# Optimization experiments

Hardware: AMD Instinct MI355X
Metric: run time of the kernel (lower is better)

## Reference

```python
import jax, jax.numpy as jnp
import numpy as np

NUM_Q_HEADS = 32
NUM_KV_HEADS = 8
HEAD_DIM = 128
ROPE_THETA = 10000.0
Q_SIZE = NUM_Q_HEADS * HEAD_DIM      # 4096
KV_SIZE = NUM_KV_HEADS * HEAD_DIM    # 1024


def _apply_rope_neox(x, positions, theta=ROPE_THETA):
    # x: [T, H, D]; neox-style rotate-halves RoPE
    T, H, D = x.shape
    half = D // 2
    inv_freq = 1.0 / (theta ** (jnp.arange(half, dtype=jnp.float32) / half))
    freqs = positions.astype(jnp.float32)[:, None] * inv_freq[None, :]  # [T, half]
    cos = jnp.cos(freqs)[:, None, :]  # [T, 1, half]
    sin = jnp.sin(freqs)[:, None, :]
    x1, x2 = x[..., :half], x[..., half:]
    return jnp.concatenate([x1 * cos - x2 * sin, x2 * cos + x1 * sin], axis=-1).astype(x.dtype)


def setup_inputs() -> dict:
    key = jax.random.key(0)
    k1, k2, k3 = jax.random.split(key, 3)
    T, E = 8192, 4096
    hidden_states = jax.random.normal(k1, (T, E), dtype=jnp.float32) * 0.02
    positions = jnp.arange(T, dtype=jnp.int32)
    w_qkv = jax.random.normal(k2, (E, Q_SIZE + 2 * KV_SIZE), dtype=jnp.float32) * 0.02
    w_o = jax.random.normal(k3, (Q_SIZE, E), dtype=jnp.float32) * 0.02
    return {"hidden_states": hidden_states, "positions": positions, "w_qkv": w_qkv, "w_o": w_o}


def reference(hidden_states, positions, w_qkv, w_o):
    T = hidden_states.shape[0]
    qkv = hidden_states @ w_qkv                              # [T, 6144]
    q = qkv[:, :Q_SIZE].reshape(T, NUM_Q_HEADS, HEAD_DIM)
    k = qkv[:, Q_SIZE:Q_SIZE + KV_SIZE].reshape(T, NUM_KV_HEADS, HEAD_DIM)
    v = qkv[:, Q_SIZE + KV_SIZE:]                            # [T, KV_SIZE] (unused by stub)
    q = _apply_rope_neox(q, positions)
    k = _apply_rope_neox(k, positions)
    # Attention is stubbed in the source (randn_like(q)); we use the RoPE'd q
    # as the deterministic stand-in so the pipeline stays reproducible.
    attn_output = q.reshape(T, Q_SIZE)
    output = attn_output @ w_o                               # [T, 4096]
    return output
```

## Files before the change

### kernel.cpp

```cpp
#include <hip/hip_runtime.h>
#include <hip/hip_bf16.h>
#include <stdint.h>

#define T_DIM 8192
#define E_DIM 4096
#define NQH   32
#define HD    128
#define QSZ   (NQH * HD)
#define QKV_COLS 6144

typedef unsigned short u16;
typedef __attribute__((ext_vector_type(8))) short   bf16x8;
typedef __attribute__((ext_vector_type(4))) float   f32x4;
typedef __attribute__((ext_vector_type(4))) unsigned short u16x4;

__device__ __forceinline__ u16 f2bf(float f) {
    uint32_t u = __float_as_uint(f);
    u += 0x7fffu + ((u >> 16) & 1u);
    return (u16)(u >> 16);
}
__device__ __forceinline__ float bf2f(u16 u) {
    return __uint_as_float(((uint32_t)u) << 16);
}

__device__ __forceinline__ void gload_lds16(u16* lds, const u16* g) {
    __builtin_amdgcn_global_load_lds(
        (const __attribute__((address_space(1))) uint32_t*)g,
        (__attribute__((address_space(3))) uint32_t*)lds,
        16, 0, 0);
}

__global__ void convert_f32_bf16(const float* __restrict__ in, u16* __restrict__ out, size_t n4) {
    size_t i = (size_t)blockIdx.x * blockDim.x + threadIdx.x;
    size_t stride = (size_t)gridDim.x * blockDim.x;
    for (; i < n4; i += stride) {
        float4 v = ((const float4*)in)[i];
        u16x4 o;
        o.x = f2bf(v.x); o.y = f2bf(v.y); o.z = f2bf(v.z); o.w = f2bf(v.w);
        ((u16x4*)out)[i] = o;
    }
}

__global__ void transpose_conv(const float* __restrict__ W, u16* __restrict__ Wt,
                               int K, int N, int ldW, int colOff) {
    __shared__ float tile[32][33];
    const int tx = threadIdx.x, ty = threadIdx.y;
    const int n0 = blockIdx.x * 32, k0 = blockIdx.y * 32;
#pragma unroll
    for (int j = 0; j < 4; ++j) {
        int k = k0 + ty + j * 8;
        tile[ty + j * 8][tx] = W[(size_t)k * ldW + colOff + n0 + tx];
    }
    __syncthreads();
#pragma unroll
    for (int j = 0; j < 4; ++j) {
        int n = n0 + ty + j * 8;
        Wt[(size_t)n * K + k0 + tx] = f2bf(tile[tx][ty + j * 8]);
    }
}

__global__ void rope_table(const int* __restrict__ pos, float2* __restrict__ tab) {
    int idx = blockIdx.x * blockDim.x + threadIdx.x;
    int t = idx >> 6, d = idx & 63;
    float inv = powf(10000.0f, -(float)d * (1.0f / 64.0f));
    float fr  = (float)pos[t] * inv;
    float s, c;
    sincosf(fr, &s, &c);
    tab[idx] = make_float2(c, s);
}

__device__ __forceinline__ void store_out(u16* p, float v)  { *p = f2bf(v); }
__device__ __forceinline__ void store_out(float* p, float v){ *p = v; }

#define VMC(N)  asm volatile("s_waitcnt vmcnt(%0)"  :: "n"(N) : "memory")
#define LGKM(N) asm volatile("s_waitcnt lgkmcnt(%0)" :: "n"(N) : "memory")
#define PHASE_SYNC() do { __builtin_amdgcn_sched_barrier(0); __builtin_amdgcn_s_barrier(); \
                          LGKM(0); __builtin_amdgcn_sched_barrier(0); } while (0)
#define ENDBAR() do { __builtin_amdgcn_sched_barrier(0); __builtin_amdgcn_s_barrier(); } while (0)

#define STG_A(buf, h, kOff) do { \
    const u16* s_ = sA + (size_t)(h) * 128 * K + (kOff); \
    u16* d_ = dL + (buf) * 32768 + (h) * 8192; \
    gload_lds16(d_, s_); gload_lds16(d_ + 4096, s_ + (size_t)64 * K); } while (0)
#define STG_B(buf, h, kOff) do { \
    const u16* s_ = sB + (size_t)(h) * 128 * K + (kOff); \
    u16* d_ = dL + 16384 + (buf) * 32768 + (h) * 8192; \
    gload_lds16(d_, s_); gload_lds16(d_ + 4096, s_ + (size_t)64 * K); } while (0)

#define RD_A(buf, miBase, d0, d1) do { _Pragma("unroll") \
    for (int m = 0; m < 4; ++m) { \
        const u16* p_ = lds + (buf) * 32768 + wm * 8192 + ((miBase) + m) * 1024 + aRow; \
        d0[m] = *(const bf16x8*)(p_ + cOf0); \
        d1[m] = *(const bf16x8*)(p_ + cOf1); } } while (0)
#define RD_B(buf, niBase, d0, d1) do { _Pragma("unroll") \
    for (int n = 0; n < 2; ++n) { \
        const int ni_ = (niBase) + n; \
        const u16* p_ = lds + (buf) * 32768 + 16384 + (ni_ >> 1) * 8192 + \
                        ((ni_ & 1) * 64 + wn * 16) * 64 + aRow; \
        d0[n] = *(const bf16x8*)(p_ + cOf0); \
        d1[n] = *(const bf16x8*)(p_ + cOf1); } } while (0)

#define MM(miBase, niBase, A0, A1, B0, B1) do { \
    __builtin_amdgcn_s_setprio(1); \
    _Pragma("unroll") for (int m = 0; m < 4; ++m) \
    _Pragma("unroll") for (int n = 0; n < 2; ++n) { \
        acc[(miBase) + m][(niBase) + n] = __builtin_amdgcn_mfma_f32_16x16x32_bf16( \
            A0[m], B0[n], acc[(miBase) + m][(niBase) + n], 0, 0, 0); \
        acc[(miBase) + m][(niBase) + n] = __builtin_amdgcn_mfma_f32_16x16x32_bf16( \
            A1[m], B1[n], acc[(miBase) + m][(niBase) + n], 0, 0, 0); } \
    __builtin_amdgcn_s_setprio(0); } while (0)

#define TILE(BUF, KN) do {                                                     \
                                                                  \
    RD_A(BUF, 0, a0K0, a0K1);                                                  \
    RD_B(BUF, 0, b01K0, b01K1);                                                \
    STG_A((BUF) ^ 1, 0, KN);                                                   \
    LGKM(8);                                                                   \
    PHASE_SYNC();                                                              \
    MM(0, 0, a0K0, a0K1, b01K0, b01K1);                                        \
    ENDBAR();                                                                  \
                                                                  \
    RD_A(BUF, 4, a4K0, a4K1);                                                  \
    STG_A((BUF) ^ 1, 1, KN);                                                   \
    VMC(4);                                                                    \
    PHASE_SYNC();                                                              \
    MM(4, 0, a4K0, a4K1, b01K0, b01K1);                                        \
    ENDBAR();                                                                  \
                                                                  \
    RD_B(BUF, 2, b23K0, b23K1);                                                \
    STG_B((BUF) ^ 1, 0, KN);                                                   \
    PHASE_SYNC();                                                              \
    MM(0, 2, a0K0, a0K1, b23K0, b23K1);                                        \
    ENDBAR();                                                                  \
                                                                  \
    STG_B((BUF) ^ 1, 1, KN);                                                   \
    VMC(2);                                                                    \
    PHASE_SYNC();                                                              \
    MM(4, 2, a4K0, a4K1, b23K0, b23K1);                                        \
    ENDBAR();                                                                  \
  } while (0)

template <typename OutT, bool ROPE>
__global__ __launch_bounds__(512, 2) void gemm256(const u16* __restrict__ A,
                                                  const u16* __restrict__ Bt,
                                                  OutT* __restrict__ C,
                                                  const float2* __restrict__ tab,
                                                  int M, int N, int K) {
    __shared__ u16 lds[65536];
    const int tid  = threadIdx.x;
    const int lane = tid & 63;
    const int wid  = tid >> 6;
    const int wm = wid >> 2;
    const int wn = wid & 3;
    const int lr  = lane & 15;
    const int kq  = lane >> 4;
    const int lr7 = lr & 7;
    const int aRow = lr * 64;
    const int cOf0 = ((kq) ^ lr7) << 3;
    const int cOf1 = ((4 + kq) ^ lr7) << 3;

    const int nwg = gridDim.x;
    const int cpx = nwg >> 3;
    const int bid = blockIdx.x;
    const int swz = (bid & 7) * cpx + (bid >> 3);
    const int numM = M >> 8;
    const size_t rowBase = (size_t)(swz % numM) << 8;
    const size_t colBase = (size_t)(swz / numM) << 8;

    const int r0 = tid >> 3;
    const int cS = (((tid & 7) ^ (r0 & 7)) << 3);
    const u16* sA = A  + (rowBase + r0) * (size_t)K + cS;
    const u16* sB = Bt + (colBase + r0) * (size_t)K + cS;
    u16* dL = &lds[0] + tid * 8;

    f32x4 acc[8][4];
#pragma unroll
    for (int i = 0; i < 8; ++i)
#pragma unroll
        for (int j = 0; j < 4; ++j)
            acc[i][j] = (f32x4){0.f, 0.f, 0.f, 0.f};

    bf16x8 a0K0[4], a0K1[4], a4K0[4], a4K1[4];
    bf16x8 b01K0[2], b01K1[2], b23K0[2], b23K1[2];

    STG_A(0, 0, 0); STG_A(0, 1, 0); STG_B(0, 0, 0);
    STG_B(0, 1, 0);
    VMC(2);
    __builtin_amdgcn_sched_barrier(0);
    __builtin_amdgcn_s_barrier();
    __builtin_amdgcn_sched_barrier(0);

    const int nT = K >> 6;
    for (int t = 0; t < nT; t += 2) {
        const int kN1 = (t + 1) << 6;
        const int kN2 = (t + 2 < nT) ? ((t + 2) << 6) : 0;
        TILE(0, kN1);
        TILE(1, kN2);
    }
    VMC(0);

    if constexpr (ROPE) {
        const int dIdx = wn * 16 + lr;
#pragma unroll
        for (int mi = 0; mi < 8; ++mi)
#pragma unroll
            for (int r = 0; r < 4; ++r) {
                size_t row = rowBase + wm * 128 + mi * 16 + (kq << 2) + r;
                float2 cs = tab[row * 64 + dIdx];
#pragma unroll
                for (int hp = 0; hp < 2; ++hp) {
                    float x1 = acc[mi][hp * 2 + 0][r];
                    float x2 = acc[mi][hp * 2 + 1][r];
                    size_t c1 = colBase + hp * 128 + wn * 16 + lr;
                    C[row * (size_t)N + c1]      = f2bf(x1 * cs.x - x2 * cs.y);
                    C[row * (size_t)N + c1 + 64] = f2bf(x2 * cs.x + x1 * cs.y);
                }
            }
    } else {
#pragma unroll
        for (int mi = 0; mi < 8; ++mi)
#pragma unroll
            for (int ni = 0; ni < 4; ++ni)
#pragma unroll
                for (int r = 0; r < 4; ++r) {
                    size_t row = rowBase + wm * 128 + mi * 16 + (kq << 2) + r;
                    size_t col = colBase + ni * 64 + wn * 16 + lr;
                    store_out(&C[row * (size_t)N + col], acc[mi][ni][r]);
                }
    }
}

extern "C" void kernel_launch(void* const* d_in, const int* in_sizes, int n_in,
                              void* d_out, int out_size, void* d_ws, size_t ws_size,
                              hipStream_t stream) {
    const float* hidden    = (const float*)d_in[0];
    const int*   positions = (const int*)d_in[1];
    const float* w_qkv     = (const float*)d_in[2];
    const float* w_o       = (const float*)d_in[3];
    float* out = (float*)d_out;

    u16* Hb  = (u16*)d_ws;
    u16* WqT = Hb  + (size_t)T_DIM * E_DIM;
    u16* WoT = WqT + (size_t)QSZ * E_DIM;
    u16* Qb  = WoT + (size_t)E_DIM * QSZ;
    float2* tab = (float2*)WoT;

    convert_f32_bf16<<<2048, 256, 0, stream>>>(hidden, Hb, (size_t)T_DIM * E_DIM / 4);

    dim3 tb(32, 8);
    transpose_conv<<<dim3(QSZ / 32, E_DIM / 32), tb, 0, stream>>>(w_qkv, WqT, E_DIM, QSZ, QKV_COLS, 0);
    rope_table<<<(T_DIM * 64) / 256, 256, 0, stream>>>(positions, tab);

    gemm256<u16, true><<<dim3((T_DIM / 256) * (QSZ / 256)), 512, 0, stream>>>(
        Hb, WqT, Qb, tab, T_DIM, QSZ, E_DIM);

    transpose_conv<<<dim3(E_DIM / 32, QSZ / 32), tb, 0, stream>>>(w_o, WoT, QSZ, E_DIM, E_DIM, 0);

    gemm256<float, false><<<dim3((T_DIM / 256) * (E_DIM / 256)), 512, 0, stream>>>(
        Qb, WoT, out, nullptr, T_DIM, E_DIM, QSZ);
}
```

Baseline: 608.7 us.

## Restructure GEMM main loop with register-prefetched fragments and fewer barriers

Rewrites the per-tile schedule of the bf16 MFMA GEMM. The K-halves of each 64-wide tile are now split across four phases. LDS fragments for the next phase, and for the first phase of the next tile, are read into registers while the current MFMAs run. The explicit lgkmcnt waits and the paired start/end barriers are replaced by a single barrier per phase, and all global-to-LDS staging for the next buffer is issued in the first two phases. This aims to cut barrier stalls and expose more LDS/MFMA overlap, at the cost of more live fragment registers and a full vmcnt(0) drain per tile.

```diff
diff --git a/kernel.cpp b/kernel.cpp
--- a/kernel.cpp
+++ b/kernel.cpp
@@ -73,10 +73,9 @@
 __device__ __forceinline__ void store_out(float* p, float v){ *p = v; }
 
 #define VMC(N)  asm volatile("s_waitcnt vmcnt(%0)"  :: "n"(N) : "memory")
-#define LGKM(N) asm volatile("s_waitcnt lgkmcnt(%0)" :: "n"(N) : "memory")
-#define PHASE_SYNC() do { __builtin_amdgcn_sched_barrier(0); __builtin_amdgcn_s_barrier(); \
-                          LGKM(0); __builtin_amdgcn_sched_barrier(0); } while (0)
-#define ENDBAR() do { __builtin_amdgcn_sched_barrier(0); __builtin_amdgcn_s_barrier(); } while (0)
+#define BARS()  do { __builtin_amdgcn_sched_barrier(0); __builtin_amdgcn_s_barrier(); } while (0)
+#define BARSPUB() do { __builtin_amdgcn_sched_barrier(0); __builtin_amdgcn_s_barrier(); \
+                       __builtin_amdgcn_sched_barrier(0); } while (0)
 
 #define STG_A(buf, h, kOff) do { \
     const u16* s_ = sA + (size_t)(h) * 128 * K + (kOff); \
@@ -87,57 +86,45 @@
     u16* d_ = dL + 16384 + (buf) * 32768 + (h) * 8192; \
     gload_lds16(d_, s_); gload_lds16(d_ + 4096, s_ + (size_t)64 * K); } while (0)
 
-#define RD_A(buf, miBase, d0, d1) do { _Pragma("unroll") \
+#define RD_A4(buf, miBase, OF, dst) do { _Pragma("unroll") \
     for (int m = 0; m < 4; ++m) { \
-        const u16* p_ = lds + (buf) * 32768 + wm * 8192 + ((miBase) + m) * 1024 + aRow; \
-        d0[m] = *(const bf16x8*)(p_ + cOf0); \
-        d1[m] = *(const bf16x8*)(p_ + cOf1); } } while (0)
-#define RD_B(buf, niBase, d0, d1) do { _Pragma("unroll") \
-    for (int n = 0; n < 2; ++n) { \
-        const int ni_ = (niBase) + n; \
-        const u16* p_ = lds + (buf) * 32768 + 16384 + (ni_ >> 1) * 8192 + \
-                        ((ni_ & 1) * 64 + wn * 16) * 64 + aRow; \
-        d0[n] = *(const bf16x8*)(p_ + cOf0); \
-        d1[n] = *(const bf16x8*)(p_ + cOf1); } } while (0)
-
-#define MM(miBase, niBase, A0, A1, B0, B1) do { \
+        dst[m] = *(const bf16x8*)&lds[(buf) * 32768 + wm * 8192 + \
+                                      ((miBase) + m) * 1024 + aRow + (OF)]; } } while (0)
+#define RD_B4(buf, OF, dst) do { _Pragma("unroll") \
+    for (int n = 0; n < 4; ++n) { \
+        dst[n] = *(const bf16x8*)&lds[(buf) * 32768 + 16384 + (n >> 1) * 8192 + \
+                                      ((n & 1) * 64 + wn * 16) * 64 + aRow + (OF)]; } } while (0)
+
+#define MM16(miBase, Af, Bf) do { \
     __builtin_amdgcn_s_setprio(1); \
     _Pragma("unroll") for (int m = 0; m < 4; ++m) \
-    _Pragma("unroll") for (int n = 0; n < 2; ++n) { \
-        acc[(miBase) + m][(niBase) + n] = __builtin_amdgcn_mfma_f32_16x16x32_bf16( \
-            A0[m], B0[n], acc[(miBase) + m][(niBase) + n], 0, 0, 0); \
-        acc[(miBase) + m][(niBase) + n] = __builtin_amdgcn_mfma_f32_16x16x32_bf16( \
-            A1[m], B1[n], acc[(miBase) + m][(niBase) + n], 0, 0, 0); } \
+    _Pragma("unroll") for (int n = 0; n < 4; ++n) \
+        acc[(miBase) + m][n] = __builtin_amdgcn_mfma_f32_16x16x32_bf16( \
+            Af[m], Bf[n], acc[(miBase) + m][n], 0, 0, 0); \
     __builtin_amdgcn_s_setprio(0); } while (0)
 
 #define TILE(BUF, KN) do {                                                     \
-                                                                  \
-    RD_A(BUF, 0, a0K0, a0K1);                                                  \
-    RD_B(BUF, 0, b01K0, b01K1);                                                \
-    STG_A((BUF) ^ 1, 0, KN);                                                   \
-    LGKM(8);                                                                   \
-    PHASE_SYNC();                                                              \
-    MM(0, 0, a0K0, a0K1, b01K0, b01K1);                                        \
-    ENDBAR();                                                                  \
-                                                                  \
-    RD_A(BUF, 4, a4K0, a4K1);                                                  \
-    STG_A((BUF) ^ 1, 1, KN);                                                   \
-    VMC(4);                                                                    \
-    PHASE_SYNC();                                                              \
-    MM(4, 0, a4K0, a4K1, b01K0, b01K1);                                        \
-    ENDBAR();                                                                  \
-                                                                  \
-    RD_B(BUF, 2, b23K0, b23K1);                                                \
-    STG_B((BUF) ^ 1, 0, KN);                                                   \
-    PHASE_SYNC();                                                              \
-    MM(0, 2, a0K0, a0K1, b23K0, b23K1);                                        \
-    ENDBAR();                                                                  \
-                                                                  \
-    STG_B((BUF) ^ 1, 1, KN);                                                   \
-    VMC(2);                                                                    \
-    PHASE_SYNC();                                                              \
-    MM(4, 2, a4K0, a4K1, b23K0, b23K1);                                        \
-    ENDBAR();                                                                  \
+                                                                       \
+    STG_A((BUF) ^ 1, 0, KN); STG_A((BUF) ^ 1, 1, KN);                          \
+    BARS();                                                                    \
+    RD_A4(BUF, 4, cOf0, aX);                                                   \
+    MM16(0, aC, bK0);                                                          \
+                                                                       \
+    STG_B((BUF) ^ 1, 0, KN); STG_B((BUF) ^ 1, 1, KN);                          \
+    BARS();                                                                    \
+    RD_A4(BUF, 0, cOf1, aY);                                                   \
+    RD_B4(BUF, cOf1, bK1);                                                     \
+    MM16(4, aX, bK0);                                                          \
+                                                                       \
+    BARS();                                                                    \
+    RD_A4(BUF, 4, cOf1, aZ);                                                   \
+    MM16(0, aY, bK1);                                                          \
+                                                                       \
+    VMC(0);                                                                    \
+    BARSPUB();                                                                 \
+    RD_A4((BUF) ^ 1, 0, cOf0, aC);                                             \
+    RD_B4((BUF) ^ 1, cOf0, bK0);                                               \
+    MM16(4, aZ, bK1);                                                          \
   } while (0)
 
 template <typename OutT, bool ROPE>
@@ -180,15 +167,14 @@
         for (int j = 0; j < 4; ++j)
             acc[i][j] = (f32x4){0.f, 0.f, 0.f, 0.f};
 
-    bf16x8 a0K0[4], a0K1[4], a4K0[4], a4K1[4];
-    bf16x8 b01K0[2], b01K1[2], b23K0[2], b23K1[2];
-
-    STG_A(0, 0, 0); STG_A(0, 1, 0); STG_B(0, 0, 0);
-    STG_B(0, 1, 0);
-    VMC(2);
-    __builtin_amdgcn_sched_barrier(0);
-    __builtin_amdgcn_s_barrier();
-    __builtin_amdgcn_sched_barrier(0);
+    bf16x8 aC[4], aX[4], aY[4], aZ[4];
+    bf16x8 bK0[4], bK1[4];
+
+    STG_A(0, 0, 0); STG_A(0, 1, 0); STG_B(0, 0, 0); STG_B(0, 1, 0);
+    VMC(0);
+    BARSPUB();
+    RD_A4(0, 0, cOf0, aC);
+    RD_B4(0, cOf0, bK0);
 
     const int nT = K >> 6;
     for (int t = 0; t < nT; t += 2) {
@@ -197,7 +183,6 @@
         TILE(0, kN1);
         TILE(1, kN2);
     }
-    VMC(0);
 
     if constexpr (ROPE) {
         const int dIdx = wn * 16 + lr;
```

Result: faster. 573.2 us (-5.8%).
